# Performance work log

Hardware: AMD Instinct MI355X
Metric: run time of the kernel (lower is better)

Reference implementation:

```python
import jax, jax.numpy as jnp
import numpy as np

# Staggered-grid first-derivative coefficients (Taylor-optimal), order -> c_1..c_N
_COEFFS = {2: (1.0,),
           4: (9.0 / 8.0, -1.0 / 24.0),
           6: (75.0 / 64.0, -25.0 / 384.0, 3.0 / 640.0),
           8: (1225.0 / 1024.0, -245.0 / 3072.0, 49.0 / 5120.0, -5.0 / 7168.0)}


def _shift(a, s, axis):
    """Zero-padded shift: out[i] = a[i + s] where valid, else 0."""
    if s == 0:
        return a
    nd = a.ndim
    sl = [slice(None)] * nd
    pad = [(0, 0)] * nd
    if s > 0:
        sl[axis] = slice(s, None)
        pad[axis] = (0, s)
    else:
        sl[axis] = slice(None, s)
        pad[axis] = (-s, 0)
    return jnp.pad(a[tuple(sl)], pad)


def _diff1(a, stencil, rd, axis):
    """Integer-grid staggered derivative: sum_k c_k (a[i+k-1] - a[i-k]) * rd."""
    d = jnp.zeros_like(a)
    for k, ck in enumerate(_COEFFS[stencil], start=1):
        d = d + ck * (_shift(a, k - 1, axis) - _shift(a, -k, axis))
    return d * rd


def _diffh1(a, stencil, rd, axis):
    """Half-grid staggered derivative: sum_k c_k (a[i+k] - a[i-k+1]) * rd."""
    d = jnp.zeros_like(a)
    for k, ck in enumerate(_COEFFS[stencil], start=1):
        d = d + ck * (_shift(a, k, axis) - _shift(a, -(k - 1), axis))
    return d * rd


def _step(ca, cb, cq, Ey, Hx, Hz, m_Hx_z, m_Hz_x, m_Ey_x, m_Ey_z,
          ky, ky_h, ay, ay_h, by, by_h, kx, kx_h, ax, ax_h, bx, bx_h,
          rdy, rdx, stencil):
    # ---- update_E ----
    dHz_dx = _diff1(Hz, stencil, rdx, -1)   # d/dx along last axis
    dHx_dz = _diff1(Hx, stencil, rdy, -2)   # d/dz (y) along axis -2
    m_Hz_x = bx * m_Hz_x + ax * dHz_dx
    m_Hx_z = by * m_Hx_z + ay * dHx_dz
    Ey = ca * Ey + cb * ((dHz_dx / kx + m_Hz_x) - (dHx_dz / ky + m_Hx_z))
    # ---- update_H ----
    dEy_dz = _diffh1(Ey, stencil, rdy, -2)
    dEy_dx = _diffh1(Ey, stencil, rdx, -1)
    m_Ey_z = by_h * m_Ey_z + ay_h * dEy_dz
    m_Ey_x = bx_h * m_Ey_x + ax_h * dEy_dx
    Hx = Hx - cq * (dEy_dz / ky_h + m_Ey_z)
    Hz = Hz + cq * (dEy_dx / kx_h + m_Ey_x)
    return jnp.stack([Ey, Hx, Hz, m_Hx_z, m_Hz_x, m_Ey_x, m_Ey_z])


def setup_inputs() -> dict:
    B, NY, NX = 2, 2048, 2048
    key = jax.random.key(0)
    ks = jax.random.split(key, 25)
    f32 = jnp.float32

    def rn(k, s):
        return jax.random.normal(k, s, f32)

    def ru(k, s):
        return jax.random.uniform(k, s, f32)

    inp = {
        'ca': 0.9 + 0.1 * ru(ks[0], (NY, NX)),        # ~1 (low-loss media)
        'cb': 0.1 * ru(ks[1], (NY, NX)),
        'cq': 0.1 * ru(ks[2], (NY, NX)),
        'Ey': rn(ks[3], (B, NY, NX)),
        'Hx': rn(ks[4], (B, NY, NX)),
        'Hz': rn(ks[5], (B, NY, NX)),
        'm_Hx_z': rn(ks[6], (B, NY, NX)),
        'm_Hz_x': rn(ks[7], (B, NY, NX)),
        'm_Ey_x': rn(ks[8], (B, NY, NX)),
        'm_Ey_z': rn(ks[9], (B, NY, NX)),
        'ky': 1.0 + ru(ks[10], (NY, 1)),              # kappa >= 1
        'ky_h': 1.0 + ru(ks[11], (NY, 1)),
        'ay': 0.1 * ru(ks[12], (NY, 1)),
        'ay_h': 0.1 * ru(ks[13], (NY, 1)),
        'by': 0.9 * ru(ks[14], (NY, 1)),
        'by_h': 0.9 * ru(ks[15], (NY, 1)),
        'kx': 1.0 + ru(ks[16], (NX,)),
        'kx_h': 1.0 + ru(ks[17], (NX,)),
        'ax': 0.1 * ru(ks[18], (NX,)),
        'ax_h': 0.1 * ru(ks[19], (NX,)),
        'bx': 0.9 * ru(ks[20], (NX,)),
        'bx_h': 0.9 * ru(ks[21], (NX,)),
        'rdy': jnp.float32(0.1),
        'rdx': jnp.float32(0.1),
        'stencil': 4,
    }
    return inp


def reference(ca, cb, cq, Ey, Hx, Hz, m_Hx_z, m_Hz_x, m_Ey_x, m_Ey_z,
              ky, ky_h, ay, ay_h, by, by_h, kx, kx_h, ax, ax_h, bx, bx_h,
              rdy, rdx, stencil):
    return _step(ca, cb, cq, Ey, Hx, Hz, m_Hx_z, m_Hz_x, m_Ey_x, m_Ey_z,
                 ky, ky_h, ay, ay_h, by, by_h, kx, kx_h, ax, ax_h, bx, bx_h,
                 rdy, rdx, int(stencil))
```

## Files before the change

kernel.cpp:

```cpp
#include <hip/hip_runtime.h>

typedef __attribute__((ext_vector_type(4))) float float4v;

#define TY    8
#define WXW   256
#define WXP   (WXW + 8)

__device__ __forceinline__ float4v ld4(const float* __restrict__ p) {
    return *(const float4v*)p;
}
__device__ __forceinline__ void st4(float* __restrict__ p, float4v v) {
    *(float4v*)p = v;
}
__device__ __forceinline__ float frcp(float x) {
    return __builtin_amdgcn_rcpf(x);
}

template<int NS>
__global__ __launch_bounds__(64) void fdtd_ns(
    const float* __restrict__ ca,   const float* __restrict__ cb,
    const float* __restrict__ cq,
    const float* __restrict__ Ey,   const float* __restrict__ Hx,
    const float* __restrict__ Hz,
    const float* __restrict__ mHxz, const float* __restrict__ mHzx,
    const float* __restrict__ mEyx, const float* __restrict__ mEyz,
    const float* __restrict__ ky,   const float* __restrict__ kyh,
    const float* __restrict__ ay,   const float* __restrict__ ayh,
    const float* __restrict__ by,   const float* __restrict__ byh,
    const float* __restrict__ kx,   const float* __restrict__ kxh,
    const float* __restrict__ ax,   const float* __restrict__ axh,
    const float* __restrict__ bx,   const float* __restrict__ bxh,
    const float* __restrict__ rdyp, const float* __restrict__ rdxp,
    const int* __restrict__ stp,
    float* __restrict__ outEy,   float* __restrict__ outHx,
    float* __restrict__ outHz,   float* __restrict__ outMHxz,
    float* __restrict__ outMHzx, float* __restrict__ outMEyx,
    float* __restrict__ outMEyz,
    int B, int NY, int NX, int NSTRIP, int NWX)
{
    int nsr = stp[0] >> 1;
    if (nsr < 1) nsr = 1; if (nsr > 4) nsr = 4;
    if (nsr != NS) return;

    constexpr int NSLOT = (NS <= 2) ? 4 : 8;
    __shared__ float eyl[NSLOT][WXP];

    float C[4] = {0.f, 0.f, 0.f, 0.f};
    if constexpr (NS == 1)      { C[0] = 1.f; }
    else if constexpr (NS == 2) { C[0] = 1.125f;          C[1] = -1.f/24.f; }
    else if constexpr (NS == 3) { C[0] = 75.f/64.f;       C[1] = -25.f/384.f;
                                  C[2] = 3.f/640.f; }
    else                        { C[0] = 1225.f/1024.f;   C[1] = -245.f/3072.f;
                                  C[2] = 49.f/5120.f;     C[3] = -5.f/7168.f; }

    const int nwg = NSTRIP * NWX;
    int idx = blockIdx.x;
    if ((nwg & 7) == 0) {
        const int q = nwg >> 3;
        idx = (idx & 7) * q + (idx >> 3);
    }
    const int strip = idx % NSTRIP;
    const int wx    = idx / NSTRIP;
    const int b  = blockIdx.y;
    const int y0 = strip * TY;
    const int W0 = wx * WXW;
    const int lane = (int)threadIdx.x & 63;
    const int x0  = W0 + lane * 4;
    const int lc0 = lane * 4;

    const float rdx = rdxp[0];
    const float rdy = rdyp[0];
    const size_t NXs = (size_t)NX;
    const size_t planeOff = (size_t)b * (size_t)NY * NXs;
    const float4v z4 = {0.f, 0.f, 0.f, 0.f};
    const bool inX    = (x0 + 4 <= NX);
    const bool isHalo = (lane == 0) || (lane == 63);
    const int  xh     = (lane == 0) ? (W0 - 4) : (W0 + WXW);
    const bool haloIn = isHalo && (xh >= 0) && (xh + 4 <= NX);

    float4v rkx = z4, axv = z4, bxv = z4, rkxh = z4, axhv = z4, bxhv = z4;
    if (inX) {
        float4v t = ld4(kx + x0);
        #pragma unroll
        for (int i = 0; i < 4; ++i) rkx[i] = frcp(t[i]);
        axv = ld4(ax + x0); bxv = ld4(bx + x0);
        t = ld4(kxh + x0);
        #pragma unroll
        for (int i = 0; i < 4; ++i) rkxh[i] = frcp(t[i]);
        axhv = ld4(axh + x0); bxhv = ld4(bxh + x0);
    }
    float4v rkxH = z4, axvH = z4, bxvH = z4;
    if (haloIn) {
        float4v t = ld4(kx + xh);
        #pragma unroll
        for (int i = 0; i < 4; ++i) rkxH[i] = frcp(t[i]);
        axvH = ld4(ax + xh); bxvH = ld4(bx + xh);
    }

    float4v hxr[NSLOT], hzc[NSLOT];
    #pragma unroll
    for (int j = 0; j < NSLOT; ++j) { hxr[j] = z4; hzc[j] = z4; }
    #pragma unroll
    for (int j = 0; j < 2*NS - 1; ++j) {
        const int rr = y0 + 1 - 2*NS + j;
        if (rr >= 0 && inX)
            hxr[rr & (NSLOT-1)] = ld4(Hx + planeOff + (size_t)rr * NXs + x0);
    }

    constexpr int NITER = TY + 2*NS - 1;
    constexpr int NCH   = (NITER + NSLOT - 1) / NSLOT;
    for (int mch = 0; mch < NCH; ++mch) {
        #pragma unroll
        for (int j = 0; j < NSLOT; ++j) {
            const int e = 1 - NS + mch * NSLOT + j;
            if (e > TY + NS - 1) break;
            const int r = y0 + e;
            const int h = r - NS;
            const bool rin = (r >= 0) && (r < NY);
            const bool doH = (e >= NS) && (h < NY) && inX;
            const size_t rb = planeOff + (size_t)r * NXs;

            float4v hxv = z4, hzv = z4, mxv = z4, mzv = z4, cqv = z4;
            float ayhv = 0.f, byhv = 0.f, rkyh = 0.f;
            size_t hb = 0;
            if (doH) {
                hb  = planeOff + (size_t)h * NXs;
                hxv = hxr[h & (NSLOT-1)];
                hzv = hzc[h & (NSLOT-1)];
                mxv = ld4(mEyx + hb + x0);
                mzv = ld4(mEyz + hb + x0);
                cqv = ld4(cq + (size_t)h * NXs + x0);
                ayhv = ayh[h]; byhv = byh[h]; rkyh = frcp(kyh[h]);
            }

            {
                const int rr = r + NS - 1;
                hxr[rr & (NSLOT-1)] =
                    (rr < NY && inX) ? ld4(Hx + planeOff + (size_t)rr * NXs + x0)
                                     : z4;
            }

            float ayv = 0.f, byv = 0.f, rky = 0.f;
            if (rin) { ayv = ay[r]; byv = by[r]; rky = frcp(ky[r]); }
            float4v eM = z4;
            if (rin && inX) {
                float4v l0 = (x0 >= 4)      ? ld4(Hz + rb + x0 - 4) : z4;
                float4v l1 =                  ld4(Hz + rb + x0);
                float4v l2 = (x0 + 8 <= NX) ? ld4(Hz + rb + x0 + 4) : z4;
                hzc[r & (NSLOT-1)] = l1;
                float w[12] = {l0.x,l0.y,l0.z,l0.w, l1.x,l1.y,l1.z,l1.w,
                               l2.x,l2.y,l2.z,l2.w};
                float dzx[4] = {0,0,0,0}, dxz[4] = {0,0,0,0};
                #pragma unroll
                for (int k = 1; k <= NS; ++k) {
                    const float ck = C[k-1];
                    #pragma unroll
                    for (int i = 0; i < 4; ++i)
                        dzx[i] += ck * (w[i+3+k] - w[i+4-k]);
                    float4v up = hxr[(r+k-1) & (NSLOT-1)];
                    float4v dn = hxr[(r-k)   & (NSLOT-1)];
                    #pragma unroll
                    for (int i = 0; i < 4; ++i)
                        dxz[i] += ck * (up[i] - dn[i]);
                }
                float4v eyv = ld4(Ey   + rb + x0);
                float4v mzx = ld4(mHzx + rb + x0);
                float4v mxz = ld4(mHxz + rb + x0);
                const size_t crr = (size_t)r * NXs + x0;
                float4v cav = ld4(ca + crr);
                float4v cbv = ld4(cb + crr);
                float4v oMxz, oMzx;
                #pragma unroll
                for (int i = 0; i < 4; ++i) {
                    const float dHzdx = dzx[i] * rdx;
                    const float dHxdz = dxz[i] * rdy;
                    const float mzx_n = bxv[i] * mzx[i] + axv[i] * dHzdx;
                    const float mxz_n = byv    * mxz[i] + ayv    * dHxdz;
                    eM[i] = cav[i] * eyv[i]
                          + cbv[i] * ((dHzdx * rkx[i] + mzx_n)
                                    - (dHxdz * rky    + mxz_n));
                    oMxz[i] = mxz_n; oMzx[i] = mzx_n;
                }
                if (e >= 0 && e < TY) {
                    st4(outEy   + rb + x0, eM);
                    st4(outMHxz + rb + x0, oMxz);
                    st4(outMHzx + rb + x0, oMzx);
                }
            }

            float4v eH = z4;
            if (haloIn && rin) {
                float4v l0 = (xh >= 4)      ? ld4(Hz + rb + xh - 4) : z4;
                float4v l1 =                  ld4(Hz + rb + xh);
                float4v l2 = (xh + 8 <= NX) ? ld4(Hz + rb + xh + 4) : z4;
                float w[12] = {l0.x,l0.y,l0.z,l0.w, l1.x,l1.y,l1.z,l1.w,
                               l2.x,l2.y,l2.z,l2.w};
                float dzx[4] = {0,0,0,0}, dxz[4] = {0,0,0,0};
                #pragma unroll
                for (int k = 1; k <= NS; ++k) {
                    const float ck = C[k-1];
                    #pragma unroll
                    for (int i = 0; i < 4; ++i)
                        dzx[i] += ck * (w[i+3+k] - w[i+4-k]);
                    const int yp = r + k - 1, ym = r - k;
                    float4v up = (yp < NY) ? ld4(Hx + planeOff + (size_t)yp*NXs + xh) : z4;
                    float4v dn = (ym >= 0) ? ld4(Hx + planeOff + (size_t)ym*NXs + xh) : z4;
                    #pragma unroll
                    for (int i = 0; i < 4; ++i)
                        dxz[i] += ck * (up[i] - dn[i]);
                }
                float4v eyv = ld4(Ey   + rb + xh);
                float4v mzx = ld4(mHzx + rb + xh);
                float4v mxz = ld4(mHxz + rb + xh);
                const size_t crr = (size_t)r * NXs + xh;
                float4v cav = ld4(ca + crr);
                float4v cbv = ld4(cb + crr);
                #pragma unroll
                for (int i = 0; i < 4; ++i) {
                    const float dHzdx = dzx[i] * rdx;
                    const float dHxdz = dxz[i] * rdy;
                    const float mzx_n = bxvH[i] * mzx[i] + axvH[i] * dHzdx;
                    const float mxz_n = byv     * mxz[i] + ayv     * dHxdz;
                    eH[i] = cav[i] * eyv[i]
                          + cbv[i] * ((dHzdx * rkxH[i] + mzx_n)
                                    - (dHxdz * rky     + mxz_n));
                }
            }

            const int sl = r & (NSLOT-1);
            st4(&eyl[sl][lc0 + 4], eM);
            if (lane == 0)  st4(&eyl[sl][0],       eH);
            if (lane == 63) st4(&eyl[sl][WXW + 4], eH);

            if (doH) {
                const int hs = h & (NSLOT-1);
                float4v a0 = ld4(&eyl[hs][lc0]);
                float4v a1 = ld4(&eyl[hs][lc0 + 4]);
                float4v a2 = ld4(&eyl[hs][lc0 + 8]);
                float lw[12] = {a0.x,a0.y,a0.z,a0.w, a1.x,a1.y,a1.z,a1.w,
                                a2.x,a2.y,a2.z,a2.w};
                float dEdx[4] = {0,0,0,0}, dEdz[4] = {0,0,0,0};
                #pragma unroll
                for (int k = 1; k <= NS; ++k) {
                    const float ck = C[k-1];
                    #pragma unroll
                    for (int i = 0; i < 4; ++i)
                        dEdx[i] += ck * (lw[i+4+k] - lw[i+5-k]);
                    float4v up = ld4(&eyl[(h+k)   & (NSLOT-1)][lc0 + 4]);
                    float4v dn = ld4(&eyl[(h-k+1) & (NSLOT-1)][lc0 + 4]);
                    #pragma unroll
                    for (int i = 0; i < 4; ++i)
                        dEdz[i] += ck * (up[i] - dn[i]);
                }
                float4v oHx, oHz, oMx, oMz;
                #pragma unroll
                for (int i = 0; i < 4; ++i) {
                    const float dz = dEdz[i] * rdy;
                    const float dx = dEdx[i] * rdx;
                    const float mz_n = byhv    * mzv[i] + ayhv    * dz;
                    const float mx_n = bxhv[i] * mxv[i] + axhv[i] * dx;
                    oHx[i] = hxv[i] - cqv[i] * (dz * rkyh    + mz_n);
                    oHz[i] = hzv[i] + cqv[i] * (dx * rkxh[i] + mx_n);
                    oMx[i] = mx_n; oMz[i] = mz_n;
                }
                st4(outHx   + hb + x0, oHx);
                st4(outHz   + hb + x0, oHz);
                st4(outMEyx + hb + x0, oMx);
                st4(outMEyz + hb + x0, oMz);
            }
        }
    }
}

extern "C" void kernel_launch(void* const* d_in, const int* in_sizes, int n_in,
                              void* d_out, int out_size, void* d_ws, size_t ws_size,
                              hipStream_t stream)
{
    const float* ca   = (const float*)d_in[0];
    const float* cb   = (const float*)d_in[1];
    const float* cq   = (const float*)d_in[2];
    const float* Ey   = (const float*)d_in[3];
    const float* Hx   = (const float*)d_in[4];
    const float* Hz   = (const float*)d_in[5];
    const float* mHxz = (const float*)d_in[6];
    const float* mHzx = (const float*)d_in[7];
    const float* mEyx = (const float*)d_in[8];
    const float* mEyz = (const float*)d_in[9];
    const float* ky   = (const float*)d_in[10];
    const float* kyh  = (const float*)d_in[11];
    const float* ay   = (const float*)d_in[12];
    const float* ayh  = (const float*)d_in[13];
    const float* by   = (const float*)d_in[14];
    const float* byh  = (const float*)d_in[15];
    const float* kx   = (const float*)d_in[16];
    const float* kxh  = (const float*)d_in[17];
    const float* ax   = (const float*)d_in[18];
    const float* axh  = (const float*)d_in[19];
    const float* bx   = (const float*)d_in[20];
    const float* bxh  = (const float*)d_in[21];
    const float* rdy  = (const float*)d_in[22];
    const float* rdx  = (const float*)d_in[23];
    const int*   stp  = (const int*)d_in[24];

    const int NX   = in_sizes[16];
    const int NYNX = in_sizes[0];
    const int NY   = NYNX / NX;
    const int B    = in_sizes[3] / NYNX;
    const size_t plane = (size_t)B * (size_t)NYNX;

    float* out     = (float*)d_out;
    float* outEy   = out;
    float* outHx   = out + 1 * plane;
    float* outHz   = out + 2 * plane;
    float* outMHxz = out + 3 * plane;
    float* outMHzx = out + 4 * plane;
    float* outMEyx = out + 5 * plane;
    float* outMEyz = out + 6 * plane;

    const int NSTRIP = (NY + TY - 1) / TY;
    const int NWX    = (NX + WXW - 1) / WXW;

    dim3 grid(NSTRIP * NWX, B);
    dim3 block(64);

    #define LAUNCH(NSV)                                                      \
        fdtd_ns<NSV><<<grid, block, 0, stream>>>(                            \
            ca, cb, cq, Ey, Hx, Hz, mHxz, mHzx, mEyx, mEyz,                  \
            ky, kyh, ay, ayh, by, byh, kx, kxh, ax, axh, bx, bxh,            \
            rdy, rdx, stp,                                                   \
            outEy, outHx, outHz, outMHxz, outMHzx, outMEyx, outMEyz,         \
            B, NY, NX, NSTRIP, NWX)

    LAUNCH(2);
    LAUNCH(1);
    LAUNCH(3);
    LAUNCH(4);
    #undef LAUNCH
}
```

Baseline: 499.2 us.

## Use overlapping tiles with clamped branchless loads and software-pipelined row staging

Replaces the separate halo-lane E computation with overlapping tiles: each 64-lane wave covers 256 columns but writes only the inner 248, so edge lanes act as halo without extra serial work. Global loads use clamped addresses and select-masking instead of branches. The next row's loads are software-prefetched into a staging struct while the current row computes, and the row loop is fully unrolled. The cost is about 3% redundant compute and loads from the overlap, plus higher register pressure from the prefetch stage.

```diff
diff --git a/kernel.cpp b/kernel.cpp
--- a/kernel.cpp
+++ b/kernel.cpp
@@ -3,8 +3,8 @@
 typedef __attribute__((ext_vector_type(4))) float float4v;
 
 #define TY    8
-#define WXW   256
-#define WXP   (WXW + 8)
+#define TILE  248
+#define LDSW  256
 
 __device__ __forceinline__ float4v ld4(const float* __restrict__ p) {
     return *(const float4v*)p;
@@ -14,6 +14,13 @@
 }
 __device__ __forceinline__ float frcp(float x) {
     return __builtin_amdgcn_rcpf(x);
+}
+__device__ __forceinline__ int iclamp(int v, int lo, int hi) {
+    return v < lo ? lo : (v > hi ? hi : v);
+}
+__device__ __forceinline__ float4v sel4(bool m, float4v v) {
+    const float4v z4 = {0.f, 0.f, 0.f, 0.f};
+    return m ? v : z4;
 }
 
 template<int NS>
@@ -43,15 +50,16 @@
     if (nsr != NS) return;
 
     constexpr int NSLOT = (NS <= 2) ? 4 : 8;
-    __shared__ float eyl[NSLOT][WXP];
+    constexpr int M = NSLOT - 1;
+    __shared__ float eyl[NSLOT][LDSW];
 
     float C[4] = {0.f, 0.f, 0.f, 0.f};
     if constexpr (NS == 1)      { C[0] = 1.f; }
-    else if constexpr (NS == 2) { C[0] = 1.125f;          C[1] = -1.f/24.f; }
-    else if constexpr (NS == 3) { C[0] = 75.f/64.f;       C[1] = -25.f/384.f;
+    else if constexpr (NS == 2) { C[0] = 1.125f;        C[1] = -1.f/24.f; }
+    else if constexpr (NS == 3) { C[0] = 75.f/64.f;     C[1] = -25.f/384.f;
                                   C[2] = 3.f/640.f; }
-    else                        { C[0] = 1225.f/1024.f;   C[1] = -245.f/3072.f;
-                                  C[2] = 49.f/5120.f;     C[3] = -5.f/7168.f; }
+    else                        { C[0] = 1225.f/1024.f; C[1] = -245.f/3072.f;
+                                  C[2] = 49.f/5120.f;   C[3] = -5.f/7168.f; }
 
     const int nwg = NSTRIP * NWX;
     int idx = blockIdx.x;
@@ -63,182 +71,146 @@
     const int wx    = idx / NSTRIP;
     const int b  = blockIdx.y;
     const int y0 = strip * TY;
-    const int W0 = wx * WXW;
     const int lane = (int)threadIdx.x & 63;
-    const int x0  = W0 + lane * 4;
-    const int lc0 = lane * 4;
+    const int xE  = wx * TILE + (lane - 1) * 4;
 
     const float rdx = rdxp[0];
     const float rdy = rdyp[0];
     const size_t NXs = (size_t)NX;
     const size_t planeOff = (size_t)b * (size_t)NY * NXs;
-    const float4v z4 = {0.f, 0.f, 0.f, 0.f};
-    const bool inX    = (x0 + 4 <= NX);
-    const bool isHalo = (lane == 0) || (lane == 63);
-    const int  xh     = (lane == 0) ? (W0 - 4) : (W0 + WXW);
-    const bool haloIn = isHalo && (xh >= 0) && (xh + 4 <= NX);
-
-    float4v rkx = z4, axv = z4, bxv = z4, rkxh = z4, axhv = z4, bxhv = z4;
-    if (inX) {
-        float4v t = ld4(kx + x0);
+
+    const bool mL = (xE >= 4) && (xE <= NX);
+    const bool m0 = (xE >= 0) && (xE + 4 <= NX);
+    const bool mR = (xE + 8 <= NX);
+    const int  cL = iclamp(xE - 4, 0, NX - 4);
+    const int  c0 = iclamp(xE,     0, NX - 4);
+    const int  cR = iclamp(xE + 4, 0, NX - 4);
+    const bool outOK = (lane >= 1) && (lane <= 62) && m0;
+    const int  lc = lane * 4;
+
+    float4v rkx, axv, bxv, rkxh, axhv, bxhv;
+    {
+        float4v t = ld4(kx + c0);
         #pragma unroll
         for (int i = 0; i < 4; ++i) rkx[i] = frcp(t[i]);
-        axv = ld4(ax + x0); bxv = ld4(bx + x0);
-        t = ld4(kxh + x0);
+        axv = ld4(ax + c0); bxv = ld4(bx + c0);
+        t = ld4(kxh + c0);
         #pragma unroll
         for (int i = 0; i < 4; ++i) rkxh[i] = frcp(t[i]);
-        axhv = ld4(axh + x0); bxhv = ld4(bxh + x0);
-    }
-    float4v rkxH = z4, axvH = z4, bxvH = z4;
-    if (haloIn) {
-        float4v t = ld4(kx + xh);
-        #pragma unroll
-        for (int i = 0; i < 4; ++i) rkxH[i] = frcp(t[i]);
-        axvH = ld4(ax + xh); bxvH = ld4(bx + xh);
+        axhv = ld4(axh + c0); bxhv = ld4(bxh + c0);
     }
 
     float4v hxr[NSLOT], hzc[NSLOT];
     #pragma unroll
-    for (int j = 0; j < NSLOT; ++j) { hxr[j] = z4; hzc[j] = z4; }
+    for (int j = 0; j < NSLOT; ++j) {
+        hxr[j] = sel4(false, hxr[j]); hzc[j] = sel4(false, hzc[j]);
+    }
     #pragma unroll
     for (int j = 0; j < 2*NS - 1; ++j) {
-        const int rr = y0 + 1 - 2*NS + j;
-        if (rr >= 0 && inX)
-            hxr[rr & (NSLOT-1)] = ld4(Hx + planeOff + (size_t)rr * NXs + x0);
-    }
-
-    constexpr int NITER = TY + 2*NS - 1;
-    constexpr int NCH   = (NITER + NSLOT - 1) / NSLOT;
-    for (int mch = 0; mch < NCH; ++mch) {
+        const int rr  = y0 + 1 - 2*NS + j;
+        const int rrc = iclamp(rr, 0, NY - 1);
+        hxr[(1 - 2*NS + j + 16) & M] =
+            sel4(rr >= 0 && m0, ld4(Hx + planeOff + (size_t)rrc * NXs + c0));
+    }
+
+    struct St {
+        float4v hzL, hz0, hzR, ey, mzx, mxz, cav, cbv, hxN, mxv, mzv, cqv;
+        float ayv, byv, rky, ayhv, byhv, rkyh;
+    };
+    auto stage = [&](int e, bool needH) -> St {
+        St s;
+        const int r   = y0 + e;
+        const int rcE = iclamp(r, 0, NY - 1);
+        const int rr  = r + NS - 1;
+        const int rcr = iclamp(rr, 0, NY - 1);
+        const size_t rbE = planeOff + (size_t)rcE * NXs;
+        s.hzL = sel4(mL, ld4(Hz + rbE + cL));
+        s.hz0 = sel4(m0, ld4(Hz + rbE + c0));
+        s.hzR = sel4(mR, ld4(Hz + rbE + cR));
+        s.ey  = ld4(Ey   + rbE + c0);
+        s.mzx = ld4(mHzx + rbE + c0);
+        s.mxz = ld4(mHxz + rbE + c0);
+        s.cav = ld4(ca + (size_t)rcE * NXs + c0);
+        s.cbv = ld4(cb + (size_t)rcE * NXs + c0);
+        s.hxN = sel4(m0 && rr < NY,
+                     ld4(Hx + planeOff + (size_t)rcr * NXs + c0));
+        s.ayv = ay[rcE]; s.byv = by[rcE]; s.rky = frcp(ky[rcE]);
+        if (needH) {
+            const int h   = r - NS;
+            const int rch = iclamp(h, 0, NY - 1);
+            const size_t rbH = planeOff + (size_t)rch * NXs;
+            s.mxv = ld4(mEyx + rbH + c0);
+            s.mzv = ld4(mEyz + rbH + c0);
+            s.cqv = ld4(cq + (size_t)rch * NXs + c0);
+            s.ayhv = ayh[rch]; s.byhv = byh[rch]; s.rkyh = frcp(kyh[rch]);
+        } else {
+            s.mxv = sel4(false, s.hz0); s.mzv = s.mxv; s.cqv = s.mxv;
+            s.ayhv = 0.f; s.byhv = 0.f; s.rkyh = 0.f;
+        }
+        return s;
+    };
+
+    St S = stage(1 - NS, false);
+    #pragma unroll
+    for (int e = 1 - NS; e <= TY + NS - 1; ++e) {
+        const int r = y0 + e;
+        const int h = r - NS;
+        St cur = S;
+        if (e < TY + NS - 1)
+            S = stage(e + 1, (e + 1 >= NS) && (e + 1 <= NS + TY - 1));
+
+        hxr[(e + NS - 1 + 16) & M] = cur.hxN;
+        hzc[(e + 16) & M]          = cur.hz0;
+
+        float w[12] = {cur.hzL[0], cur.hzL[1], cur.hzL[2], cur.hzL[3],
+                       cur.hz0[0], cur.hz0[1], cur.hz0[2], cur.hz0[3],
+                       cur.hzR[0], cur.hzR[1], cur.hzR[2], cur.hzR[3]};
+        float dzx[4] = {0,0,0,0}, dxz[4] = {0,0,0,0};
         #pragma unroll
-        for (int j = 0; j < NSLOT; ++j) {
-            const int e = 1 - NS + mch * NSLOT + j;
-            if (e > TY + NS - 1) break;
-            const int r = y0 + e;
-            const int h = r - NS;
-            const bool rin = (r >= 0) && (r < NY);
-            const bool doH = (e >= NS) && (h < NY) && inX;
-            const size_t rb = planeOff + (size_t)r * NXs;
-
-            float4v hxv = z4, hzv = z4, mxv = z4, mzv = z4, cqv = z4;
-            float ayhv = 0.f, byhv = 0.f, rkyh = 0.f;
-            size_t hb = 0;
-            if (doH) {
-                hb  = planeOff + (size_t)h * NXs;
-                hxv = hxr[h & (NSLOT-1)];
-                hzv = hzc[h & (NSLOT-1)];
-                mxv = ld4(mEyx + hb + x0);
-                mzv = ld4(mEyz + hb + x0);
-                cqv = ld4(cq + (size_t)h * NXs + x0);
-                ayhv = ayh[h]; byhv = byh[h]; rkyh = frcp(kyh[h]);
+        for (int k = 1; k <= NS; ++k) {
+            const float ck = C[k-1];
+            #pragma unroll
+            for (int i = 0; i < 4; ++i)
+                dzx[i] += ck * (w[i+3+k] - w[i+4-k]);
+            float4v up = hxr[(e + k - 1 + 16) & M];
+            float4v dn = hxr[(e - k + 16) & M];
+            #pragma unroll
+            for (int i = 0; i < 4; ++i)
+                dxz[i] += ck * (up[i] - dn[i]);
+        }
+        float4v eM, oMxz, oMzx;
+        #pragma unroll
+        for (int i = 0; i < 4; ++i) {
+            const float dHzdx = dzx[i] * rdx;
+            const float dHxdz = dxz[i] * rdy;
+            const float mzx_n = bxv[i]  * cur.mzx[i] + axv[i]  * dHzdx;
+            const float mxz_n = cur.byv * cur.mxz[i] + cur.ayv * dHxdz;
+            eM[i] = cur.cav[i] * cur.ey[i]
+                  + cur.cbv[i] * ((dHzdx * rkx[i]  + mzx_n)
+                                - (dHxdz * cur.rky + mxz_n));
+            oMxz[i] = mxz_n; oMzx[i] = mzx_n;
+        }
+        const bool rin = (r >= 0) && (r < NY);
+        eM = sel4(rin && m0, eM);
+        if (e >= 0 && e < TY) {
+            if (rin && outOK) {
+                const size_t rb = planeOff + (size_t)r * NXs;
+                st4(outEy   + rb + xE, eM);
+                st4(outMHxz + rb + xE, oMxz);
+                st4(outMHzx + rb + xE, oMzx);
             }
-
-            {
-                const int rr = r + NS - 1;
-                hxr[rr & (NSLOT-1)] =
-                    (rr < NY && inX) ? ld4(Hx + planeOff + (size_t)rr * NXs + x0)
-                                     : z4;
-            }
-
-            float ayv = 0.f, byv = 0.f, rky = 0.f;
-            if (rin) { ayv = ay[r]; byv = by[r]; rky = frcp(ky[r]); }
-            float4v eM = z4;
-            if (rin && inX) {
-                float4v l0 = (x0 >= 4)      ? ld4(Hz + rb + x0 - 4) : z4;
-                float4v l1 =                  ld4(Hz + rb + x0);
-                float4v l2 = (x0 + 8 <= NX) ? ld4(Hz + rb + x0 + 4) : z4;
-                hzc[r & (NSLOT-1)] = l1;
-                float w[12] = {l0.x,l0.y,l0.z,l0.w, l1.x,l1.y,l1.z,l1.w,
-                               l2.x,l2.y,l2.z,l2.w};
-                float dzx[4] = {0,0,0,0}, dxz[4] = {0,0,0,0};
-                #pragma unroll
-                for (int k = 1; k <= NS; ++k) {
-                    const float ck = C[k-1];
-                    #pragma unroll
-                    for (int i = 0; i < 4; ++i)
-                        dzx[i] += ck * (w[i+3+k] - w[i+4-k]);
-                    float4v up = hxr[(r+k-1) & (NSLOT-1)];
-                    float4v dn = hxr[(r-k)   & (NSLOT-1)];
-                    #pragma unroll
-                    for (int i = 0; i < 4; ++i)
-                        dxz[i] += ck * (up[i] - dn[i]);
-                }
-                float4v eyv = ld4(Ey   + rb + x0);
-                float4v mzx = ld4(mHzx + rb + x0);
-                float4v mxz = ld4(mHxz + rb + x0);
-                const size_t crr = (size_t)r * NXs + x0;
-                float4v cav = ld4(ca + crr);
-                float4v cbv = ld4(cb + crr);
-                float4v oMxz, oMzx;
-                #pragma unroll
-                for (int i = 0; i < 4; ++i) {
-                    const float dHzdx = dzx[i] * rdx;
-                    const float dHxdz = dxz[i] * rdy;
-                    const float mzx_n = bxv[i] * mzx[i] + axv[i] * dHzdx;
-                    const float mxz_n = byv    * mxz[i] + ayv    * dHxdz;
-                    eM[i] = cav[i] * eyv[i]
-                          + cbv[i] * ((dHzdx * rkx[i] + mzx_n)
-                                    - (dHxdz * rky    + mxz_n));
-                    oMxz[i] = mxz_n; oMzx[i] = mzx_n;
-                }
-                if (e >= 0 && e < TY) {
-                    st4(outEy   + rb + x0, eM);
-                    st4(outMHxz + rb + x0, oMxz);
-                    st4(outMHzx + rb + x0, oMzx);
-                }
-            }
-
-            float4v eH = z4;
-            if (haloIn && rin) {
-                float4v l0 = (xh >= 4)      ? ld4(Hz + rb + xh - 4) : z4;
-                float4v l1 =                  ld4(Hz + rb + xh);
-                float4v l2 = (xh + 8 <= NX) ? ld4(Hz + rb + xh + 4) : z4;
-                float w[12] = {l0.x,l0.y,l0.z,l0.w, l1.x,l1.y,l1.z,l1.w,
-                               l2.x,l2.y,l2.z,l2.w};
-                float dzx[4] = {0,0,0,0}, dxz[4] = {0,0,0,0};
-                #pragma unroll
-                for (int k = 1; k <= NS; ++k) {
-                    const float ck = C[k-1];
-                    #pragma unroll
-                    for (int i = 0; i < 4; ++i)
-                        dzx[i] += ck * (w[i+3+k] - w[i+4-k]);
-                    const int yp = r + k - 1, ym = r - k;
-                    float4v up = (yp < NY) ? ld4(Hx + planeOff + (size_t)yp*NXs + xh) : z4;
-                    float4v dn = (ym >= 0) ? ld4(Hx + planeOff + (size_t)ym*NXs + xh) : z4;
-                    #pragma unroll
-                    for (int i = 0; i < 4; ++i)
-                        dxz[i] += ck * (up[i] - dn[i]);
-                }
-                float4v eyv = ld4(Ey   + rb + xh);
-                float4v mzx = ld4(mHzx + rb + xh);
-                float4v mxz = ld4(mHxz + rb + xh);
-                const size_t crr = (size_t)r * NXs + xh;
-                float4v cav = ld4(ca + crr);
-                float4v cbv = ld4(cb + crr);
-                #pragma unroll
-                for (int i = 0; i < 4; ++i) {
-                    const float dHzdx = dzx[i] * rdx;
-                    const float dHxdz = dxz[i] * rdy;
-                    const float mzx_n = bxvH[i] * mzx[i] + axvH[i] * dHzdx;
-                    const float mxz_n = byv     * mxz[i] + ayv     * dHxdz;
-                    eH[i] = cav[i] * eyv[i]
-                          + cbv[i] * ((dHzdx * rkxH[i] + mzx_n)
-                                    - (dHxdz * rky     + mxz_n));
-                }
-            }
-
-            const int sl = r & (NSLOT-1);
-            st4(&eyl[sl][lc0 + 4], eM);
-            if (lane == 0)  st4(&eyl[sl][0],       eH);
-            if (lane == 63) st4(&eyl[sl][WXW + 4], eH);
-
-            if (doH) {
-                const int hs = h & (NSLOT-1);
-                float4v a0 = ld4(&eyl[hs][lc0]);
-                float4v a1 = ld4(&eyl[hs][lc0 + 4]);
-                float4v a2 = ld4(&eyl[hs][lc0 + 8]);
-                float lw[12] = {a0.x,a0.y,a0.z,a0.w, a1.x,a1.y,a1.z,a1.w,
-                                a2.x,a2.y,a2.z,a2.w};
+        }
+
+        st4(&eyl[(e + 16) & M][lc], eM);
+
+        if (e >= NS) {
+            if (h < NY && outOK) {
+                float4v a0 = ld4(&eyl[(e - NS + 16) & M][lc - 4]);
+                float4v a1 = ld4(&eyl[(e - NS + 16) & M][lc]);
+                float4v a2 = ld4(&eyl[(e - NS + 16) & M][lc + 4]);
+                float lw[12] = {a0[0],a0[1],a0[2],a0[3],
+                                a1[0],a1[1],a1[2],a1[3],
+                                a2[0],a2[1],a2[2],a2[3]};
                 float dEdx[4] = {0,0,0,0}, dEdz[4] = {0,0,0,0};
                 #pragma unroll
                 for (int k = 1; k <= NS; ++k) {
@@ -246,27 +218,30 @@
                     #pragma unroll
                     for (int i = 0; i < 4; ++i)
                         dEdx[i] += ck * (lw[i+4+k] - lw[i+5-k]);
-                    float4v up = ld4(&eyl[(h+k)   & (NSLOT-1)][lc0 + 4]);
-                    float4v dn = ld4(&eyl[(h-k+1) & (NSLOT-1)][lc0 + 4]);
+                    float4v up = ld4(&eyl[(e - NS + k + 16) & M][lc]);
+                    float4v dn = ld4(&eyl[(e - NS - k + 1 + 16) & M][lc]);
                     #pragma unroll
                     for (int i = 0; i < 4; ++i)
                         dEdz[i] += ck * (up[i] - dn[i]);
                 }
+                float4v hxv = hxr[(e - NS + 16) & M];
+                float4v hzv = hzc[(e - NS + 16) & M];
+                const size_t hb = planeOff + (size_t)h * NXs;
                 float4v oHx, oHz, oMx, oMz;
                 #pragma unroll
                 for (int i = 0; i < 4; ++i) {
                     const float dz = dEdz[i] * rdy;
                     const float dx = dEdx[i] * rdx;
-                    const float mz_n = byhv    * mzv[i] + ayhv    * dz;
-                    const float mx_n = bxhv[i] * mxv[i] + axhv[i] * dx;
-                    oHx[i] = hxv[i] - cqv[i] * (dz * rkyh    + mz_n);
-                    oHz[i] = hzv[i] + cqv[i] * (dx * rkxh[i] + mx_n);
+                    const float mz_n = cur.byhv * cur.mzv[i] + cur.ayhv * dz;
+                    const float mx_n = bxhv[i]  * cur.mxv[i] + axhv[i]  * dx;
+                    oHx[i] = hxv[i] - cur.cqv[i] * (dz * cur.rkyh + mz_n);
+                    oHz[i] = hzv[i] + cur.cqv[i] * (dx * rkxh[i]  + mx_n);
                     oMx[i] = mx_n; oMz[i] = mz_n;
                 }
-                st4(outHx   + hb + x0, oHx);
-                st4(outHz   + hb + x0, oHz);
-                st4(outMEyx + hb + x0, oMx);
-                st4(outMEyz + hb + x0, oMz);
+                st4(outHx   + hb + xE, oHx);
+                st4(outHz   + hb + xE, oHz);
+                st4(outMEyx + hb + xE, oMx);
+                st4(outMEyz + hb + xE, oMz);
             }
         }
     }
@@ -318,7 +293,7 @@
     float* outMEyz = out + 6 * plane;
 
     const int NSTRIP = (NY + TY - 1) / TY;
-    const int NWX    = (NX + WXW - 1) / WXW;
+    const int NWX    = (NX + TILE - 1) / TILE;
 
     dim3 grid(NSTRIP * NWX, B);
     dim3 block(64);
```

Measured after the change: 510.3 us. 1.02x slower.
